# Optimization experiments

Measured on AMD Instinct MI355X. Metric: run time of the kernel, lower is better.

The kernel has to match this reference:

```python
import jax, jax.numpy as jnp
import numpy as np
import math

C = 1024
H = 16
D = C // H
R = 4  # max_relative_position (window_size)


def setup_inputs() -> dict:
    key = jax.random.key(0)
    ks = jax.random.split(key, 10)
    B, S = 2, 2048
    scale = 1.0 / math.sqrt(C)
    inp = {
        "x": jax.random.normal(ks[0], (B, S, C), dtype=jnp.float32),
        "mask": jnp.ones((B, 1, 1, S), dtype=jnp.int32),
        "Wq": jax.random.normal(ks[1], (C, C), dtype=jnp.float32) * scale,
        "bq": jnp.zeros((C,), dtype=jnp.float32),
        "Wk": jax.random.normal(ks[2], (C, C), dtype=jnp.float32) * scale,
        "bk": jnp.zeros((C,), dtype=jnp.float32),
        "Wv": jax.random.normal(ks[3], (C, C), dtype=jnp.float32) * scale,
        "bv": jnp.zeros((C,), dtype=jnp.float32),
        "Wo": jax.random.normal(ks[4], (C, C), dtype=jnp.float32) * scale,
        "bo": jnp.zeros((C,), dtype=jnp.float32),
        "rel_key": jax.random.normal(ks[5], (2 * R + 1, D), dtype=jnp.float32) * 0.02,
    }
    return inp


def reference(x, mask, Wq, bq, Wk, bk, Wv, bv, Wo, bo, rel_key):
    B, S, Cc = x.shape
    inv = 1.0 / math.sqrt(D)
    # projections -> [B, H, S, D]
    q = (x @ Wq.T + bq).reshape(B, S, H, D).transpose(0, 2, 1, 3)
    k = (x @ Wk.T + bk).reshape(B, S, H, D).transpose(0, 2, 1, 3)
    v = (x @ Wv.T + bv).reshape(B, S, H, D).transpose(0, 2, 1, 3)
    scores = jnp.einsum("bhqd,bhkd->bhqk", q, k) * inv
    # relative position bias: positions[q,k] in [0, 2R]
    pos = jnp.clip(jnp.arange(S)[None, :] - jnp.arange(S)[:, None], -R, R) + R
    # project q onto the small rel table first ([B,H,S,2R+1]), then gather per (q,k)
    proj = jnp.einsum("bhqd,rd->bhqr", q, rel_key) * inv
    rel_scores = proj[:, :, jnp.arange(S)[:, None], pos]  # [B,H,S,S]
    scores = scores + rel_scores
    scores = jnp.where(mask == 0, jnp.float32(-1e9), scores)
    attn = jax.nn.softmax(scores, axis=-1)
    out = jnp.einsum("bhqk,bhkd->bhqd", attn, v)
    out = out.transpose(0, 2, 1, 3).reshape(B, S, Cc)
    return out @ Wo.T + bo
```

## Files before the change

### kernel.cpp

```cpp
#include <hip/hip_runtime.h>
#include <math.h>

#define B_ 2
#define S_ 2048
#define C_ 1024
#define H_ 16
#define D_ 64

typedef _Float16 f16;
typedef _Float16 half8 __attribute__((ext_vector_type(8)));
typedef _Float16 half4v __attribute__((ext_vector_type(4)));
typedef float floatx4 __attribute__((ext_vector_type(4)));

#define LD4F(p) (*reinterpret_cast<const float4*>(p))
#define LD16U(p) (*reinterpret_cast<const uint4*>(p))

__global__ __launch_bounds__(256)
void convert_inputs(const float* __restrict__ x,
                    const float* __restrict__ Wq, const float* __restrict__ Wk,
                    const float* __restrict__ Wv, const float* __restrict__ Wo,
                    f16* __restrict__ dst)
{
    const size_t XN = (size_t)B_ * S_ * C_;
    const size_t WN = (size_t)C_ * C_;
    size_t i = (size_t)blockIdx.x * 256 + threadIdx.x;
    size_t e = i * 4;
    if (e >= XN + 4 * WN) return;
    const float* s; size_t o;
    if (e < XN) { s = x; o = e; }
    else {
        size_t j = e - XN;
        int w = (int)(j >> 20);
        s = (w == 0) ? Wq : (w == 1) ? Wk : (w == 2) ? Wv : Wo;
        o = j & (WN - 1);
    }
    float4 val = LD4F(&s[o]);
    half4v hv;
    hv[0] = (f16)val.x; hv[1] = (f16)val.y; hv[2] = (f16)val.z; hv[3] = (f16)val.w;
    *reinterpret_cast<half4v*>(&dst[e]) = hv;
}

__global__ __launch_bounds__(256)
void qkv_gemm_h(const f16* __restrict__ xh, const f16* __restrict__ Wbase,
                const float* __restrict__ bq, const float* __restrict__ bk,
                const float* __restrict__ bv,
                f16* __restrict__ qo, f16* __restrict__ ko, f16* __restrict__ vo)
{
    const int which = blockIdx.z;
    const f16* W      = Wbase + (size_t)which * C_ * C_;
    const float* bias = (which == 0) ? bq : (which == 1) ? bk : bv;
    f16* out          = (which == 0) ? qo : (which == 1) ? ko : vo;

    const int mb = blockIdx.x * 128;
    const int nb = blockIdx.y * 128;
    const int tid = threadIdx.x;
    const int lane = tid & 63;
    const int wid = tid >> 6;
    const int wr = wid >> 1, wc = wid & 1;
    const int l15 = lane & 15, g = lane >> 4;

    __shared__ __align__(16) f16 As[128 * 40];
    __shared__ __align__(16) f16 Bs[128 * 40];

    floatx4 acc[4][4];
#pragma unroll
    for (int m = 0; m < 4; ++m)
#pragma unroll
        for (int n = 0; n < 4; ++n) acc[m][n] = (floatx4){0.f, 0.f, 0.f, 0.f};

    for (int k0 = 0; k0 < C_; k0 += 32) {
        uint4 ra[2], rb[2];
#pragma unroll
        for (int p = 0; p < 2; ++p) {
            int idx = tid + 256 * p;
            int row = idx >> 2, c4 = idx & 3;
            ra[p] = LD16U(&xh[(size_t)(mb + row) * C_ + k0 + c4 * 8]);
            rb[p] = LD16U(&W [(size_t)(nb + row) * C_ + k0 + c4 * 8]);
        }
        __syncthreads();
#pragma unroll
        for (int p = 0; p < 2; ++p) {
            int idx = tid + 256 * p;
            int row = idx >> 2, c4 = idx & 3;
            *reinterpret_cast<uint4*>(&As[row * 40 + c4 * 8]) = ra[p];
            *reinterpret_cast<uint4*>(&Bs[row * 40 + c4 * 8]) = rb[p];
        }
        __syncthreads();

        half8 af[4];
#pragma unroll
        for (int m = 0; m < 4; ++m)
            af[m] = *reinterpret_cast<const half8*>(&As[(wr * 64 + m * 16 + l15) * 40 + g * 8]);
#pragma unroll
        for (int n = 0; n < 4; ++n) {
            half8 bf = *reinterpret_cast<const half8*>(&Bs[(wc * 64 + n * 16 + l15) * 40 + g * 8]);
#pragma unroll
            for (int m = 0; m < 4; ++m)
                acc[m][n] = __builtin_amdgcn_mfma_f32_16x16x32_f16(af[m], bf, acc[m][n], 0, 0, 0);
        }
    }

#pragma unroll
    for (int n = 0; n < 4; ++n) {
        int col = nb + wc * 64 + n * 16 + l15;
        float bb = bias[col];
        int h = col >> 6, d = col & 63;
#pragma unroll
        for (int m = 0; m < 4; ++m)
#pragma unroll
            for (int r = 0; r < 4; ++r) {
                int row = mb + wr * 64 + m * 16 + g * 4 + r;
                int b = row >> 11, s = row & (S_ - 1);
                out[(((size_t)b * H_ + h) * S_ + s) * D_ + d] = (f16)(acc[m][n][r] + bb);
            }
    }
}

__global__ __launch_bounds__(256)
void attn_mfma(const f16* __restrict__ q, const f16* __restrict__ k,
               const f16* __restrict__ v, const int* __restrict__ mask,
               const float* __restrict__ rel, f16* __restrict__ ctx)
{
    const int qb = blockIdx.x * 64;
    const int bh = blockIdx.y;
    const int b = bh >> 4, h = bh & 15;
    const f16* qh_ = q + (size_t)bh * S_ * D_;
    const f16* kh_ = k + (size_t)bh * S_ * D_;
    const f16* vh_ = v + (size_t)bh * S_ * D_;

    const int tid = threadIdx.x;
    const int lane = tid & 63;
    const int wid = tid >> 6;
    const int l15 = lane & 15, g = lane >> 4;

    __shared__ __align__(16) f16 Ks[64 * 72];
    __shared__ __align__(16) f16 Vs[64 * 68];
    __shared__ __align__(16) f16 Ps[4][16 * 72];
    __shared__ float Prj[64][12];

    const int qrow = qb + wid * 16 + l15;
    half8 aq0 = *reinterpret_cast<const half8*>(&qh_[(size_t)qrow * D_ + g * 8]);
    half8 aq1 = *reinterpret_cast<const half8*>(&qh_[(size_t)qrow * D_ + 32 + g * 8]);

#pragma unroll
    for (int rr = 0; rr < 9; ++rr) {
        float p = 0.f;
#pragma unroll
        for (int j = 0; j < 8; ++j) {
            p += (float)aq0[j] * rel[rr * D_ + g * 8 + j];
            p += (float)aq1[j] * rel[rr * D_ + 32 + g * 8 + j];
        }
        p += __shfl_xor(p, 16);
        p += __shfl_xor(p, 32);
        if (lane < 16) Prj[wid * 16 + l15][rr] = p * 0.125f;
    }

    floatx4 o[4];
    float mrun[4], lrun[4];
#pragma unroll
    for (int n = 0; n < 4; ++n) o[n] = (floatx4){0.f, 0.f, 0.f, 0.f};
#pragma unroll
    for (int r = 0; r < 4; ++r) { mrun[r] = -INFINITY; lrun[r] = 0.f; }

    for (int jt = 0; jt < S_ / 64; ++jt) {
        const int jb = jt * 64;
        uint4 kr[2], vr[2];
#pragma unroll
        for (int p = 0; p < 2; ++p) {
            int idx = tid + 256 * p;
            int row = idx >> 3, c8 = idx & 7;
            kr[p] = LD16U(&kh_[(size_t)(jb + row) * D_ + c8 * 8]);
            vr[p] = LD16U(&vh_[(size_t)(jb + row) * D_ + c8 * 8]);
        }
        __syncthreads();
#pragma unroll
        for (int p = 0; p < 2; ++p) {
            int idx = tid + 256 * p;
            int row = idx >> 3, c8 = idx & 7;
            *reinterpret_cast<uint4*>(&Ks[row * 72 + c8 * 8]) = kr[p];
            const uint2* vv = reinterpret_cast<const uint2*>(&vr[p]);
            *reinterpret_cast<uint2*>(&Vs[row * 68 + c8 * 8]) = vv[0];
            *reinterpret_cast<uint2*>(&Vs[row * 68 + c8 * 8 + 4]) = vv[1];
        }
        __syncthreads();

        floatx4 sc[4];
#pragma unroll
        for (int n = 0; n < 4; ++n) sc[n] = (floatx4){0.f, 0.f, 0.f, 0.f};
#pragma unroll
        for (int n = 0; n < 4; ++n) {
            half8 bk0 = *reinterpret_cast<const half8*>(&Ks[(n * 16 + l15) * 72 + g * 8]);
            half8 bk1 = *reinterpret_cast<const half8*>(&Ks[(n * 16 + l15) * 72 + 32 + g * 8]);
            sc[n] = __builtin_amdgcn_mfma_f32_16x16x32_f16(aq0, bk0, sc[n], 0, 0, 0);
            sc[n] = __builtin_amdgcn_mfma_f32_16x16x32_f16(aq1, bk1, sc[n], 0, 0, 0);
        }

        float pvv[4][4];
#pragma unroll
        for (int n = 0; n < 4; ++n) {
            int jg = jb + n * 16 + l15;
            int mv = mask[b * S_ + jg];
#pragma unroll
            for (int r = 0; r < 4; ++r) {
                int ig = qb + wid * 16 + g * 4 + r;
                int dp = jg - ig;
                dp = dp < -4 ? -4 : (dp > 4 ? 4 : dp);
                float val = sc[n][r] * 0.125f + Prj[wid * 16 + g * 4 + r][dp + 4];
                pvv[n][r] = mv ? val : -1.0e9f;
            }
        }

#pragma unroll
        for (int r = 0; r < 4; ++r) {
            float mx = fmaxf(fmaxf(pvv[0][r], pvv[1][r]), fmaxf(pvv[2][r], pvv[3][r]));
            mx = fmaxf(mx, __shfl_xor(mx, 1));
            mx = fmaxf(mx, __shfl_xor(mx, 2));
            mx = fmaxf(mx, __shfl_xor(mx, 4));
            mx = fmaxf(mx, __shfl_xor(mx, 8));
            float mnew = fmaxf(mrun[r], mx);
            float scl = __expf(mrun[r] - mnew);
            float rs = 0.f;
#pragma unroll
            for (int n = 0; n < 4; ++n) {
                float e = __expf(pvv[n][r] - mnew);
                pvv[n][r] = e; rs += e;
            }
            rs += __shfl_xor(rs, 1); rs += __shfl_xor(rs, 2);
            rs += __shfl_xor(rs, 4); rs += __shfl_xor(rs, 8);
            lrun[r] = lrun[r] * scl + rs;
            mrun[r] = mnew;
#pragma unroll
            for (int n = 0; n < 4; ++n) o[n][r] *= scl;
        }

#pragma unroll
        for (int n = 0; n < 4; ++n)
#pragma unroll
            for (int r = 0; r < 4; ++r)
                Ps[wid][(g * 4 + r) * 72 + n * 16 + l15] = (f16)pvv[n][r];

        half8 pa0 = *reinterpret_cast<const half8*>(&Ps[wid][l15 * 72 + g * 8]);
        half8 pa1 = *reinterpret_cast<const half8*>(&Ps[wid][l15 * 72 + 32 + g * 8]);

#pragma unroll
        for (int n = 0; n < 4; ++n) {
            half8 bv0, bv1;
            int kv0 = g * 8;
#pragma unroll
            for (int j = 0; j < 8; ++j)
                bv0[j] = Vs[(kv0 + j) * 68 + n * 16 + l15];
#pragma unroll
            for (int j = 0; j < 8; ++j)
                bv1[j] = Vs[(32 + kv0 + j) * 68 + n * 16 + l15];
            o[n] = __builtin_amdgcn_mfma_f32_16x16x32_f16(pa0, bv0, o[n], 0, 0, 0);
            o[n] = __builtin_amdgcn_mfma_f32_16x16x32_f16(pa1, bv1, o[n], 0, 0, 0);
        }
    }

#pragma unroll
    for (int n = 0; n < 4; ++n) {
        int dcol = n * 16 + l15;
#pragma unroll
        for (int r = 0; r < 4; ++r) {
            int srow = qb + wid * 16 + g * 4 + r;
            float val = o[n][r] / lrun[r];
            ctx[((size_t)(b * S_ + srow)) * C_ + h * D_ + dcol] = (f16)val;
        }
    }
}

__global__ __launch_bounds__(256)
void out_gemm_h(const f16* __restrict__ A, const f16* __restrict__ W,
                const float* __restrict__ bias, float* __restrict__ out)
{
    const int mb = blockIdx.x * 128;
    const int nb = blockIdx.y * 128;
    const int tid = threadIdx.x;
    const int lane = tid & 63;
    const int wid = tid >> 6;
    const int wr = wid >> 1, wc = wid & 1;
    const int l15 = lane & 15, g = lane >> 4;

    __shared__ __align__(16) f16 As[128 * 40];
    __shared__ __align__(16) f16 Bs[128 * 40];

    floatx4 acc[4][4];
#pragma unroll
    for (int m = 0; m < 4; ++m)
#pragma unroll
        for (int n = 0; n < 4; ++n) acc[m][n] = (floatx4){0.f, 0.f, 0.f, 0.f};

    for (int k0 = 0; k0 < C_; k0 += 32) {
        uint4 ra[2], rb[2];
#pragma unroll
        for (int p = 0; p < 2; ++p) {
            int idx = tid + 256 * p;
            int row = idx >> 2, c4 = idx & 3;
            ra[p] = LD16U(&A[(size_t)(mb + row) * C_ + k0 + c4 * 8]);
            rb[p] = LD16U(&W[(size_t)(nb + row) * C_ + k0 + c4 * 8]);
        }
        __syncthreads();
#pragma unroll
        for (int p = 0; p < 2; ++p) {
            int idx = tid + 256 * p;
            int row = idx >> 2, c4 = idx & 3;
            *reinterpret_cast<uint4*>(&As[row * 40 + c4 * 8]) = ra[p];
            *reinterpret_cast<uint4*>(&Bs[row * 40 + c4 * 8]) = rb[p];
        }
        __syncthreads();

        half8 af[4];
#pragma unroll
        for (int m = 0; m < 4; ++m)
            af[m] = *reinterpret_cast<const half8*>(&As[(wr * 64 + m * 16 + l15) * 40 + g * 8]);
#pragma unroll
        for (int n = 0; n < 4; ++n) {
            half8 bf = *reinterpret_cast<const half8*>(&Bs[(wc * 64 + n * 16 + l15) * 40 + g * 8]);
#pragma unroll
            for (int m = 0; m < 4; ++m)
                acc[m][n] = __builtin_amdgcn_mfma_f32_16x16x32_f16(af[m], bf, acc[m][n], 0, 0, 0);
        }
    }

#pragma unroll
    for (int n = 0; n < 4; ++n) {
        int col = nb + wc * 64 + n * 16 + l15;
        float bb = bias[col];
#pragma unroll
        for (int m = 0; m < 4; ++m)
#pragma unroll
            for (int r = 0; r < 4; ++r) {
                size_t row = mb + wr * 64 + m * 16 + g * 4 + r;
                out[row * C_ + col] = acc[m][n][r] + bb;
            }
    }
}

extern "C" void kernel_launch(void* const* d_in, const int* in_sizes, int n_in,
                              void* d_out, int out_size, void* d_ws, size_t ws_size,
                              hipStream_t stream)
{
    const float* x    = (const float*)d_in[0];
    const int*   mask = (const int*)  d_in[1];
    const float* Wq   = (const float*)d_in[2];
    const float* bq   = (const float*)d_in[3];
    const float* Wk   = (const float*)d_in[4];
    const float* bk   = (const float*)d_in[5];
    const float* Wv   = (const float*)d_in[6];
    const float* bv   = (const float*)d_in[7];
    const float* Wo   = (const float*)d_in[8];
    const float* bo   = (const float*)d_in[9];
    const float* rel  = (const float*)d_in[10];
    float* out = (float*)d_out;

    const size_t XN = (size_t)B_ * S_ * C_;
    const size_t WN = (size_t)C_ * C_;

    f16* wsh  = (f16*)d_ws;
    f16* xh   = wsh;
    f16* Wqh  = wsh + XN;
    f16* Woh  = Wqh + 3 * WN;
    f16* qh   = wsh + XN + 4 * WN;
    f16* kh   = qh + XN;
    f16* vh   = kh + XN;
    f16* ctxh = vh + XN;

    convert_inputs<<<8192, 256, 0, stream>>>(x, Wq, Wk, Wv, Wo, wsh);
    qkv_gemm_h<<<dim3(32, 8, 3), 256, 0, stream>>>(xh, Wqh, bq, bk, bv, qh, kh, vh);
    attn_mfma<<<dim3(S_ / 64, B_ * H_), 256, 0, stream>>>(qh, kh, vh, mask, rel, ctxh);
    out_gemm_h<<<dim3(32, 8), 256, 0, stream>>>(ctxh, Woh, bo, out);
}
```

Baseline: 436.9 us.

## Use direct global-to-LDS loads, fold softmax scale into Q, transpose V tile

The GEMM kernels now load tiles with global_load_lds straight into unpadded LDS, which drops the register staging. Q is prescaled by log2(e)/8 so attention can use exp2 and skip the per-score multiply. V is stored transposed in LDS so the PV operands become vector loads instead of scalar gathers. Off-diagonal tiles use a precomputed constant relative bias, and the grid is remapped to group heads per XCD. The risks are LDS bank conflicts from the unpadded layout and from the transposed V stores, plus fp16 rounding of the scaled Q.

```diff
diff --git a/kernel.cpp b/kernel.cpp
--- a/kernel.cpp
+++ b/kernel.cpp
@@ -1,5 +1,4 @@
 #include <hip/hip_runtime.h>
-#include <math.h>
 
 #define B_ 2
 #define S_ 2048
@@ -14,6 +13,13 @@
 
 #define LD4F(p) (*reinterpret_cast<const float4*>(p))
 #define LD16U(p) (*reinterpret_cast<const uint4*>(p))
+#define EXP2F(x) __builtin_amdgcn_exp2f(x)
+
+__device__ __forceinline__ void gload16(const f16* g, f16* l) {
+    __builtin_amdgcn_global_load_lds(
+        (const __attribute__((address_space(1))) void*)g,
+        (__attribute__((address_space(3))) void*)l, 16, 0, 0);
+}
 
 __global__ __launch_bounds__(256)
 void convert_inputs(const float* __restrict__ x,
@@ -50,6 +56,7 @@
     const f16* W      = Wbase + (size_t)which * C_ * C_;
     const float* bias = (which == 0) ? bq : (which == 1) ? bk : bv;
     f16* out          = (which == 0) ? qo : (which == 1) ? ko : vo;
+    const float qscale = (which == 0) ? 0.18033688f : 1.0f;
 
     const int mb = blockIdx.x * 128;
     const int nb = blockIdx.y * 128;
@@ -59,8 +66,8 @@
     const int wr = wid >> 1, wc = wid & 1;
     const int l15 = lane & 15, g = lane >> 4;
 
-    __shared__ __align__(16) f16 As[128 * 40];
-    __shared__ __align__(16) f16 Bs[128 * 40];
+    __shared__ __align__(16) f16 As[128 * 32];
+    __shared__ __align__(16) f16 Bs[128 * 32];
 
     floatx4 acc[4][4];
 #pragma unroll
@@ -69,31 +76,23 @@
         for (int n = 0; n < 4; ++n) acc[m][n] = (floatx4){0.f, 0.f, 0.f, 0.f};
 
     for (int k0 = 0; k0 < C_; k0 += 32) {
-        uint4 ra[2], rb[2];
+        __syncthreads();
 #pragma unroll
         for (int p = 0; p < 2; ++p) {
-            int idx = tid + 256 * p;
-            int row = idx >> 2, c4 = idx & 3;
-            ra[p] = LD16U(&xh[(size_t)(mb + row) * C_ + k0 + c4 * 8]);
-            rb[p] = LD16U(&W [(size_t)(nb + row) * C_ + k0 + c4 * 8]);
-        }
-        __syncthreads();
-#pragma unroll
-        for (int p = 0; p < 2; ++p) {
-            int idx = tid + 256 * p;
-            int row = idx >> 2, c4 = idx & 3;
-            *reinterpret_cast<uint4*>(&As[row * 40 + c4 * 8]) = ra[p];
-            *reinterpret_cast<uint4*>(&Bs[row * 40 + c4 * 8]) = rb[p];
+            int i2 = tid + 256 * p;
+            int row = i2 >> 2, c4 = i2 & 3;
+            gload16(&xh[(size_t)(mb + row) * C_ + k0 + c4 * 8], &As[i2 * 8]);
+            gload16(&W [(size_t)(nb + row) * C_ + k0 + c4 * 8], &Bs[i2 * 8]);
         }
         __syncthreads();
 
         half8 af[4];
 #pragma unroll
         for (int m = 0; m < 4; ++m)
-            af[m] = *reinterpret_cast<const half8*>(&As[(wr * 64 + m * 16 + l15) * 40 + g * 8]);
+            af[m] = *reinterpret_cast<const half8*>(&As[(wr * 64 + m * 16 + l15) * 32 + g * 8]);
 #pragma unroll
         for (int n = 0; n < 4; ++n) {
-            half8 bf = *reinterpret_cast<const half8*>(&Bs[(wc * 64 + n * 16 + l15) * 40 + g * 8]);
+            half8 bf = *reinterpret_cast<const half8*>(&Bs[(wc * 64 + n * 16 + l15) * 32 + g * 8]);
 #pragma unroll
             for (int m = 0; m < 4; ++m)
                 acc[m][n] = __builtin_amdgcn_mfma_f32_16x16x32_f16(af[m], bf, acc[m][n], 0, 0, 0);
@@ -111,7 +110,7 @@
             for (int r = 0; r < 4; ++r) {
                 int row = mb + wr * 64 + m * 16 + g * 4 + r;
                 int b = row >> 11, s = row & (S_ - 1);
-                out[(((size_t)b * H_ + h) * S_ + s) * D_ + d] = (f16)(acc[m][n][r] + bb);
+                out[(((size_t)b * H_ + h) * S_ + s) * D_ + d] = (f16)((acc[m][n][r] + bb) * qscale);
             }
     }
 }
@@ -121,8 +120,11 @@
                const f16* __restrict__ v, const int* __restrict__ mask,
                const float* __restrict__ rel, f16* __restrict__ ctx)
 {
-    const int qb = blockIdx.x * 64;
-    const int bh = blockIdx.y;
+    const int flat = blockIdx.y * 32 + blockIdx.x;
+    const int c = flat & 7, j = flat >> 3;
+    const int bh = (c << 2) | (j >> 5);
+    const int qb = (j & 31) * 64;
+
     const int b = bh >> 4, h = bh & 15;
     const f16* qh_ = q + (size_t)bh * S_ * D_;
     const f16* kh_ = k + (size_t)bh * S_ * D_;
@@ -134,7 +136,7 @@
     const int l15 = lane & 15, g = lane >> 4;
 
     __shared__ __align__(16) f16 Ks[64 * 72];
-    __shared__ __align__(16) f16 Vs[64 * 68];
+    __shared__ __align__(16) f16 Vt[64 * 72];
     __shared__ __align__(16) f16 Ps[4][16 * 72];
     __shared__ float Prj[64][12];
 
@@ -146,13 +148,20 @@
     for (int rr = 0; rr < 9; ++rr) {
         float p = 0.f;
 #pragma unroll
-        for (int j = 0; j < 8; ++j) {
-            p += (float)aq0[j] * rel[rr * D_ + g * 8 + j];
-            p += (float)aq1[j] * rel[rr * D_ + 32 + g * 8 + j];
+        for (int jj = 0; jj < 8; ++jj) {
+            p += (float)aq0[jj] * rel[rr * D_ + g * 8 + jj];
+            p += (float)aq1[jj] * rel[rr * D_ + 32 + g * 8 + jj];
         }
         p += __shfl_xor(p, 16);
         p += __shfl_xor(p, 32);
-        if (lane < 16) Prj[wid * 16 + l15][rr] = p * 0.125f;
+        if (lane < 16) Prj[wid * 16 + l15][rr] = p;
+    }
+
+    float prj_lo[4], prj_hi[4];
+#pragma unroll
+    for (int r = 0; r < 4; ++r) {
+        prj_lo[r] = Prj[wid * 16 + g * 4 + r][0];
+        prj_hi[r] = Prj[wid * 16 + g * 4 + r][8];
     }
 
     floatx4 o[4];
@@ -178,9 +187,12 @@
             int idx = tid + 256 * p;
             int row = idx >> 3, c8 = idx & 7;
             *reinterpret_cast<uint4*>(&Ks[row * 72 + c8 * 8]) = kr[p];
-            const uint2* vv = reinterpret_cast<const uint2*>(&vr[p]);
-            *reinterpret_cast<uint2*>(&Vs[row * 68 + c8 * 8]) = vv[0];
-            *reinterpret_cast<uint2*>(&Vs[row * 68 + c8 * 8 + 4]) = vv[1];
+            const f16* vp = reinterpret_cast<const f16*>(&vr[p]);
+#pragma unroll
+            for (int jj = 0; jj < 8; ++jj) {
+                int dd = (jj + c8) & 7;
+                Vt[(c8 * 8 + dd) * 72 + row] = vp[dd];
+            }
         }
         __syncthreads();
 
@@ -196,17 +208,29 @@
         }
 
         float pvv[4][4];
-#pragma unroll
-        for (int n = 0; n < 4; ++n) {
-            int jg = jb + n * 16 + l15;
-            int mv = mask[b * S_ + jg];
-#pragma unroll
-            for (int r = 0; r < 4; ++r) {
-                int ig = qb + wid * 16 + g * 4 + r;
-                int dp = jg - ig;
-                dp = dp < -4 ? -4 : (dp > 4 ? 4 : dp);
-                float val = sc[n][r] * 0.125f + Prj[wid * 16 + g * 4 + r][dp + 4];
-                pvv[n][r] = mv ? val : -1.0e9f;
+        const bool diag = (jb >= qb - 64) && (jb <= qb + 64);
+        if (!diag) {
+            const float* pb = (jb > qb) ? prj_hi : prj_lo;
+#pragma unroll
+            for (int n = 0; n < 4; ++n) {
+                int mv = mask[b * S_ + jb + n * 16 + l15];
+#pragma unroll
+                for (int r = 0; r < 4; ++r)
+                    pvv[n][r] = mv ? (sc[n][r] + pb[r]) : -1.0e9f;
+            }
+        } else {
+#pragma unroll
+            for (int n = 0; n < 4; ++n) {
+                int jg = jb + n * 16 + l15;
+                int mv = mask[b * S_ + jg];
+#pragma unroll
+                for (int r = 0; r < 4; ++r) {
+                    int ig = qb + wid * 16 + g * 4 + r;
+                    int dp = jg - ig;
+                    dp = dp < -4 ? -4 : (dp > 4 ? 4 : dp);
+                    float val = sc[n][r] + Prj[wid * 16 + g * 4 + r][dp + 4];
+                    pvv[n][r] = mv ? val : -1.0e9f;
+                }
             }
         }
 
@@ -218,11 +242,11 @@
             mx = fmaxf(mx, __shfl_xor(mx, 4));
             mx = fmaxf(mx, __shfl_xor(mx, 8));
             float mnew = fmaxf(mrun[r], mx);
-            float scl = __expf(mrun[r] - mnew);
+            float scl = EXP2F(mrun[r] - mnew);
             float rs = 0.f;
 #pragma unroll
             for (int n = 0; n < 4; ++n) {
-                float e = __expf(pvv[n][r] - mnew);
+                float e = EXP2F(pvv[n][r] - mnew);
                 pvv[n][r] = e; rs += e;
             }
             rs += __shfl_xor(rs, 1); rs += __shfl_xor(rs, 2);
@@ -244,14 +268,8 @@
 
 #pragma unroll
         for (int n = 0; n < 4; ++n) {
-            half8 bv0, bv1;
-            int kv0 = g * 8;
-#pragma unroll
-            for (int j = 0; j < 8; ++j)
-                bv0[j] = Vs[(kv0 + j) * 68 + n * 16 + l15];
-#pragma unroll
-            for (int j = 0; j < 8; ++j)
-                bv1[j] = Vs[(32 + kv0 + j) * 68 + n * 16 + l15];
+            half8 bv0 = *reinterpret_cast<const half8*>(&Vt[(n * 16 + l15) * 72 + g * 8]);
+            half8 bv1 = *reinterpret_cast<const half8*>(&Vt[(n * 16 + l15) * 72 + 32 + g * 8]);
             o[n] = __builtin_amdgcn_mfma_f32_16x16x32_f16(pa0, bv0, o[n], 0, 0, 0);
             o[n] = __builtin_amdgcn_mfma_f32_16x16x32_f16(pa1, bv1, o[n], 0, 0, 0);
         }
@@ -281,8 +299,8 @@
     const int wr = wid >> 1, wc = wid & 1;
     const int l15 = lane & 15, g = lane >> 4;
 
-    __shared__ __align__(16) f16 As[128 * 40];
-    __shared__ __align__(16) f16 Bs[128 * 40];
+    __shared__ __align__(16) f16 As[128 * 32];
+    __shared__ __align__(16) f16 Bs[128 * 32];
 
     floatx4 acc[4][4];
 #pragma unroll
@@ -291,31 +309,23 @@
         for (int n = 0; n < 4; ++n) acc[m][n] = (floatx4){0.f, 0.f, 0.f, 0.f};
 
     for (int k0 = 0; k0 < C_; k0 += 32) {
-        uint4 ra[2], rb[2];
+        __syncthreads();
 #pragma unroll
         for (int p = 0; p < 2; ++p) {
-            int idx = tid + 256 * p;
-            int row = idx >> 2, c4 = idx & 3;
-            ra[p] = LD16U(&A[(size_t)(mb + row) * C_ + k0 + c4 * 8]);
-            rb[p] = LD16U(&W[(size_t)(nb + row) * C_ + k0 + c4 * 8]);
-        }
-        __syncthreads();
-#pragma unroll
-        for (int p = 0; p < 2; ++p) {
-            int idx = tid + 256 * p;
-            int row = idx >> 2, c4 = idx & 3;
-            *reinterpret_cast<uint4*>(&As[row * 40 + c4 * 8]) = ra[p];
-            *reinterpret_cast<uint4*>(&Bs[row * 40 + c4 * 8]) = rb[p];
+            int i2 = tid + 256 * p;
+            int row = i2 >> 2, c4 = i2 & 3;
+            gload16(&A[(size_t)(mb + row) * C_ + k0 + c4 * 8], &As[i2 * 8]);
+            gload16(&W[(size_t)(nb + row) * C_ + k0 + c4 * 8], &Bs[i2 * 8]);
         }
         __syncthreads();
 
         half8 af[4];
 #pragma unroll
         for (int m = 0; m < 4; ++m)
-            af[m] = *reinterpret_cast<const half8*>(&As[(wr * 64 + m * 16 + l15) * 40 + g * 8]);
+            af[m] = *reinterpret_cast<const half8*>(&As[(wr * 64 + m * 16 + l15) * 32 + g * 8]);
 #pragma unroll
         for (int n = 0; n < 4; ++n) {
-            half8 bf = *reinterpret_cast<const half8*>(&Bs[(wc * 64 + n * 16 + l15) * 40 + g * 8]);
+            half8 bf = *reinterpret_cast<const half8*>(&Bs[(wc * 64 + n * 16 + l15) * 32 + g * 8]);
 #pragma unroll
             for (int m = 0; m < 4; ++m)
                 acc[m][n] = __builtin_amdgcn_mfma_f32_16x16x32_f16(af[m], bf, acc[m][n], 0, 0, 0);
@@ -367,6 +377,6 @@
 
     convert_inputs<<<8192, 256, 0, stream>>>(x, Wq, Wk, Wv, Wo, wsh);
     qkv_gemm_h<<<dim3(32, 8, 3), 256, 0, stream>>>(xh, Wqh, bq, bk, bv, qh, kh, vh);
-    attn_mfma<<<dim3(S_ / 64, B_ * H_), 256, 0, stream>>>(qh, kh, vh, mask, rel, ctxh);
+    attn_mfma<<<dim3(32, 32), 256, 0, stream>>>(qh, kh, vh, mask, rel, ctxh);
     out_gemm_h<<<dim3(32, 8), 256, 0, stream>>>(ctxh, Woh, bo, out);
 }
```

New measurement: 388.5 us. 1.12x faster.
